# Kernel tuning notes

Hardware: AMD Instinct MI355X
Metric: run time of the kernel (lower is better)

The kernel has to match this reference:

```python
import jax, jax.numpy as jnp
import numpy as np

# Block-structured decompression constants (SFACTOR=2 on 32x32 channels)
RBLKS, CBLKS = 2, 2      # blocks per axis
RPIX, CPIX = 8, 8        # compressed block size
OUT_HW = 32              # decompressed channel size
B = 32768


def setup_inputs() -> dict:
    key = jax.random.key(0)
    k1, k2, k3, k4 = jax.random.split(key, 4)
    x = jax.random.normal(k1, (B, 3, 16, 16), dtype=jnp.float32)
    # per-row-block decompression matrices: [rblks, 2*RPIX, RPIX]
    lhs = jax.random.normal(k2, (RBLKS, 2 * RPIX, RPIX), dtype=jnp.float32) * 0.1
    # per-col-block decompression matrices: [cblks, CPIX, 2*CPIX]
    rhs = jax.random.normal(k3, (CBLKS, CPIX, 2 * CPIX), dtype=jnp.float32) * 0.1
    W = jax.random.normal(k4, (1, 3 * 32 * 32), dtype=jnp.float32) * 0.02
    b = jnp.zeros((1,), dtype=jnp.float32)
    return {"x": x, "lhs": lhs, "rhs": rhs, "W": W, "b": b}


def _decompress(xc, lhs, rhs):
    # xc: [B, 16, 16] compressed channel -> [B, 32, 32]
    n = xc.shape[0]
    # split into [B, rblk, RPIX, cblk, CPIX] blocks
    blocks = xc.reshape(n, RBLKS, RPIX, CBLKS, CPIX)
    # per-block: out_block = lhs[r] @ block @ rhs[c]  (block-wise bfloat16 decompression math)
    out = jnp.einsum('rPp,brpcq,cqQ->brPcQ', lhs, blocks, rhs)
    return out.reshape(n, OUT_HW, OUT_HW)


def reference(x, lhs, rhs, W, b):
    # three per-channel decompression calls, as in the original forward
    r = _decompress(x[:, 0], lhs, rhs)
    g = _decompress(x[:, 1], lhs, rhs)
    bch = _decompress(x[:, 2], lhs, rhs)
    out = jnp.stack((r, g, bch), axis=1)            # [B, 3, 32, 32]
    out = out.reshape(-1, 3 * 32 * 32)              # [B, 3072]
    return out @ W.T + b                            # [B, 1]
```

## Files before the change

kernel.cpp:

```cpp
#include <hip/hip_runtime.h>
#include <hip/hip_bf16.h>


#define BATCH 32768
#define ROW_F4 192
#define ROWS_PER_BLOCK 32
#define GRID_BLOCKS (BATCH / ROWS_PER_BLOCK)

__device__ __forceinline__ float dot4(const float4& a, const float4& b) {
    return a.x * b.x + a.y * b.y + a.z * b.z + a.w * b.w;
}

__device__ __forceinline__ void reduce2_store(float a0, float a1, int lane,
                                              float* __restrict__ outp,
                                              float bias) {
    a0 += __shfl_xor(a0, 1);
    a1 += __shfl_xor(a1, 1);
    float b = (lane & 1) ? a1 : a0;
    b += __shfl_xor(b, 2);
    b += __shfl_xor(b, 4);
    b += __shfl_xor(b, 8);
    b += __shfl_xor(b, 16);
    b += __shfl_xor(b, 32);
    if (lane < 2) outp[lane] = b + bias;
}

__global__ __launch_bounds__(256, 4) void fused_compressor_kernel(
        const float4* __restrict__ x4,
        const float4* __restrict__ lhs4,
        const float4* __restrict__ rhs4,
        const float4* __restrict__ W4,
        const float* __restrict__ bptr,
        float* __restrict__ out) {
    __shared__ __align__(16) float Wl[3072];
    __shared__ __align__(16) float rh[256];
    __shared__ __align__(16) float lh[256];
    __shared__ float tmp[1536];
    __shared__ __align__(16) float weff[768];

    const int tid  = threadIdx.x;
    const int lane = tid & 63;
    const int w    = tid >> 6;

    const int wrow = blockIdx.x * ROWS_PER_BLOCK + w * 8;

    const float4* xr = x4 + (size_t)wrow * ROW_F4 + lane;
    float4 xa[2][3], xb[2][3];
    #pragma unroll
    for (int r = 0; r < 2; ++r)
        #pragma unroll
        for (int k = 0; k < 3; ++k)
            xa[r][k] = xr[r * ROW_F4 + k * 64];
    #pragma unroll
    for (int r = 0; r < 2; ++r)
        #pragma unroll
        for (int k = 0; k < 3; ++k)
            xb[r][k] = xr[(2 + r) * ROW_F4 + k * 64];

    float4 wreg0 = W4[tid];
    float4 wreg1 = W4[tid + 256];
    float4 wreg2 = W4[tid + 512];
    int sidx = tid & 127;
    float4 sreg = (sidx < 64) ? rhs4[sidx] : lhs4[sidx - 64];

    reinterpret_cast<float4*>(Wl)[tid]       = wreg0;
    reinterpret_cast<float4*>(Wl)[tid + 256] = wreg1;
    reinterpret_cast<float4*>(Wl)[tid + 512] = wreg2;
    if (tid < 128) {
        if (tid < 64) reinterpret_cast<float4*>(rh)[tid] = sreg;
        else          reinterpret_cast<float4*>(lh)[tid - 64] = sreg;
    }
    __syncthreads();

    const float4* rhv = reinterpret_cast<const float4*>(rh);
    const float4* Wlv = reinterpret_cast<const float4*>(Wl);
    #pragma unroll
    for (int s = 0; s < 6; ++s) {
        int idx = tid + (s << 8);
        int ch  = idx >> 9;
        int rem = idx & 511;
        int R   = rem >> 4;
        int j   = rem & 15;
        int c   = j >> 3;
        int q   = j & 7;
        const float4* rp = rhv + c * 32 + q * 4;
        const float4* wp = Wlv + ch * 256 + R * 8 + c * 4;
        tmp[idx] = dot4(rp[0], wp[0]) + dot4(rp[1], wp[1])
                 + dot4(rp[2], wp[2]) + dot4(rp[3], wp[3]);
    }
    __syncthreads();

    #pragma unroll
    for (int s = 0; s < 3; ++s) {
        int idx = tid + (s << 8);
        int ch  = idx >> 8;
        int rem = idx & 255;
        int i   = rem >> 4;
        int j   = rem & 15;
        int r   = i >> 3;
        int p   = i & 7;
        const float* lp = lh + r * 128 + p;
        const float* tp = tmp + ch * 512 + r * 256 + j;
        float acc = 0.f;
        #pragma unroll
        for (int P = 0; P < 16; ++P) acc += lp[P * 8] * tp[P * 16];
        weff[idx] = acc;
    }
    __syncthreads();

    const float4* wv4 = reinterpret_cast<const float4*>(weff);
    const float4 wv0 = wv4[lane];
    const float4 wv1 = wv4[lane + 64];
    const float4 wv2 = wv4[lane + 128];
    const float  bias = bptr[0];

    {
        float a0 = dot4(xa[0][0], wv0) + dot4(xa[0][1], wv1) + dot4(xa[0][2], wv2);
        float a1 = dot4(xa[1][0], wv0) + dot4(xa[1][1], wv1) + dot4(xa[1][2], wv2);
        #pragma unroll
        for (int r = 0; r < 2; ++r)
            #pragma unroll
            for (int k = 0; k < 3; ++k)
                xa[r][k] = xr[(4 + r) * ROW_F4 + k * 64];
        reduce2_store(a0, a1, lane, out + wrow, bias);
    }
    {
        float a0 = dot4(xb[0][0], wv0) + dot4(xb[0][1], wv1) + dot4(xb[0][2], wv2);
        float a1 = dot4(xb[1][0], wv0) + dot4(xb[1][1], wv1) + dot4(xb[1][2], wv2);
        #pragma unroll
        for (int r = 0; r < 2; ++r)
            #pragma unroll
            for (int k = 0; k < 3; ++k)
                xb[r][k] = xr[(6 + r) * ROW_F4 + k * 64];
        reduce2_store(a0, a1, lane, out + wrow + 2, bias);
    }
    {
        float a0 = dot4(xa[0][0], wv0) + dot4(xa[0][1], wv1) + dot4(xa[0][2], wv2);
        float a1 = dot4(xa[1][0], wv0) + dot4(xa[1][1], wv1) + dot4(xa[1][2], wv2);
        reduce2_store(a0, a1, lane, out + wrow + 4, bias);
    }
    {
        float a0 = dot4(xb[0][0], wv0) + dot4(xb[0][1], wv1) + dot4(xb[0][2], wv2);
        float a1 = dot4(xb[1][0], wv0) + dot4(xb[1][1], wv1) + dot4(xb[1][2], wv2);
        reduce2_store(a0, a1, lane, out + wrow + 6, bias);
    }
}

extern "C" void kernel_launch(void* const* d_in, const int* in_sizes, int n_in,
                              void* d_out, int out_size, void* d_ws, size_t ws_size,
                              hipStream_t stream) {
    const float* x   = (const float*)d_in[0];
    const float* lhs = (const float*)d_in[1];
    const float* rhs = (const float*)d_in[2];
    const float* W   = (const float*)d_in[3];
    const float* b   = (const float*)d_in[4];
    float* out = (float*)d_out;

    fused_compressor_kernel<<<GRID_BLOCKS, 256, 0, stream>>>(
        (const float4*)x, (const float4*)lhs, (const float4*)rhs,
        (const float4*)W, b, out);
}
```

Measured before the change: 20.64 us.

## Load params via async LDS DMA and compute weights in one wave with flag

Weight and decompression-matrix staging now uses global_load_lds, direct global-to-LDS loads issued by wave 0, instead of going through registers. Wave 0 alone computes the effective weight vector. The other three waves spin on a volatile LDS flag rather than meeting at three block-wide barriers. The goal is to drop the register round-trip and the barrier costs so the x loads overlap the parameter setup. In exchange, one wave does four times the setup arithmetic on the critical path, and the waiting waves busy-spin and compete for issue slots. Correctness relies on the compiler inserting the wait for the LDS DMA before wave 0 reads the data.

Result: slower. 26.78 us (+29.7%).

```diff
diff --git a/kernel.cpp b/kernel.cpp
--- a/kernel.cpp
+++ b/kernel.cpp
@@ -7,8 +7,19 @@
 #define ROWS_PER_BLOCK 32
 #define GRID_BLOCKS (BATCH / ROWS_PER_BLOCK)
 
+#define PRM_W    0
+#define PRM_RHS  3072
+#define PRM_LHS  3328
+#define PRM_TOT  3584
+
 __device__ __forceinline__ float dot4(const float4& a, const float4& b) {
     return a.x * b.x + a.y * b.y + a.z * b.z + a.w * b.w;
+}
+
+__device__ __forceinline__ void async_lds16(const float* g, float* l) {
+    __builtin_amdgcn_global_load_lds(
+        (const __attribute__((address_space(1))) unsigned int*)g,
+        (__attribute__((address_space(3))) unsigned int*)l, 16, 0, 0);
 }
 
 __device__ __forceinline__ void reduce2_store(float a0, float a1, int lane,
@@ -25,24 +36,34 @@
     if (lane < 2) outp[lane] = b + bias;
 }
 
-__global__ __launch_bounds__(256, 4) void fused_compressor_kernel(
+__global__ __launch_bounds__(256, 4) void fused_pc_kernel(
         const float4* __restrict__ x4,
-        const float4* __restrict__ lhs4,
-        const float4* __restrict__ rhs4,
-        const float4* __restrict__ W4,
+        const float* __restrict__ lhsp,
+        const float* __restrict__ rhsp,
+        const float* __restrict__ Wp,
         const float* __restrict__ bptr,
         float* __restrict__ out) {
-    __shared__ __align__(16) float Wl[3072];
-    __shared__ __align__(16) float rh[256];
-    __shared__ __align__(16) float lh[256];
+    __shared__ __align__(16) float prm[PRM_TOT];
     __shared__ float tmp[1536];
     __shared__ __align__(16) float weff[768];
+    __shared__ int flag;
 
     const int tid  = threadIdx.x;
     const int lane = tid & 63;
     const int w    = tid >> 6;
+    const int wrow = blockIdx.x * ROWS_PER_BLOCK + w * 8;
 
-    const int wrow = blockIdx.x * ROWS_PER_BLOCK + w * 8;
+    if (tid == 0) flag = 0;
+    __syncthreads();
+
+    if (w == 0) {
+        #pragma unroll
+        for (int c = 0; c < 12; ++c)
+            async_lds16(Wp + c * 256 + lane * 4, prm + PRM_W + c * 256);
+        async_lds16(rhsp + lane * 4, prm + PRM_RHS);
+        async_lds16(lhsp + lane * 4, prm + PRM_LHS);
+    }
+    __builtin_amdgcn_sched_barrier(0);
 
     const float4* xr = x4 + (size_t)wrow * ROW_F4 + lane;
     float4 xa[2][3], xb[2][3];
@@ -56,59 +77,56 @@
         #pragma unroll
         for (int k = 0; k < 3; ++k)
             xb[r][k] = xr[(2 + r) * ROW_F4 + k * 64];
+    __builtin_amdgcn_sched_barrier(0);
 
-    float4 wreg0 = W4[tid];
-    float4 wreg1 = W4[tid + 256];
-    float4 wreg2 = W4[tid + 512];
-    int sidx = tid & 127;
-    float4 sreg = (sidx < 64) ? rhs4[sidx] : lhs4[sidx - 64];
+    volatile int* vflag = &flag;
+    const int g = lane >> 4;
+    const int j = lane & 15;
 
-    reinterpret_cast<float4*>(Wl)[tid]       = wreg0;
-    reinterpret_cast<float4*>(Wl)[tid + 256] = wreg1;
-    reinterpret_cast<float4*>(Wl)[tid + 512] = wreg2;
-    if (tid < 128) {
-        if (tid < 64) reinterpret_cast<float4*>(rh)[tid] = sreg;
-        else          reinterpret_cast<float4*>(lh)[tid - 64] = sreg;
+    if (w == 0) {
+        const float4* rhv = (const float4*)(prm + PRM_RHS);
+        const float4* Wlv = (const float4*)(prm + PRM_W);
+        const float*  lh  = prm + PRM_LHS;
+        const int c_ = j >> 3, q = j & 7;
+
+        const float4 rr0 = rhv[c_ * 32 + q * 4 + 0];
+        const float4 rr1 = rhv[c_ * 32 + q * 4 + 1];
+        const float4 rr2 = rhv[c_ * 32 + q * 4 + 2];
+        const float4 rr3 = rhv[c_ * 32 + q * 4 + 3];
+
+        #pragma unroll
+        for (int s = 0; s < 24; ++s) {
+            int v  = g + 4 * s;
+            int ch = v >> 5, R = v & 31;
+            const float4* wp = Wlv + ch * 256 + R * 8 + c_ * 4;
+            tmp[v * 16 + j] = dot4(rr0, wp[0]) + dot4(rr1, wp[1])
+                            + dot4(rr2, wp[2]) + dot4(rr3, wp[3]);
+        }
+
+        #pragma unroll
+        for (int ii = 0; ii < 4; ++ii) {
+            int i = g + 4 * ii;
+            int r = i >> 3, p = i & 7;
+            float lv[16];
+            #pragma unroll
+            for (int P = 0; P < 16; ++P) lv[P] = lh[r * 128 + P * 8 + p];
+            #pragma unroll
+            for (int ch = 0; ch < 3; ++ch) {
+                const float* tp = tmp + ch * 512 + r * 256 + j;
+                float acc = 0.f;
+                #pragma unroll
+                for (int P = 0; P < 16; ++P) acc += lv[P] * tp[P * 16];
+                weff[ch * 256 + i * 16 + j] = acc;
+            }
+        }
+        __threadfence_block();
+        if (lane == 0) *vflag = 1;
+    } else {
+        while (*vflag == 0) { }
+        __threadfence_block();
     }
-    __syncthreads();
 
-    const float4* rhv = reinterpret_cast<const float4*>(rh);
-    const float4* Wlv = reinterpret_cast<const float4*>(Wl);
-    #pragma unroll
-    for (int s = 0; s < 6; ++s) {
-        int idx = tid + (s << 8);
-        int ch  = idx >> 9;
-        int rem = idx & 511;
-        int R   = rem >> 4;
-        int j   = rem & 15;
-        int c   = j >> 3;
-        int q   = j & 7;
-        const float4* rp = rhv + c * 32 + q * 4;
-        const float4* wp = Wlv + ch * 256 + R * 8 + c * 4;
-        tmp[idx] = dot4(rp[0], wp[0]) + dot4(rp[1], wp[1])
-                 + dot4(rp[2], wp[2]) + dot4(rp[3], wp[3]);
-    }
-    __syncthreads();
-
-    #pragma unroll
-    for (int s = 0; s < 3; ++s) {
-        int idx = tid + (s << 8);
-        int ch  = idx >> 8;
-        int rem = idx & 255;
-        int i   = rem >> 4;
-        int j   = rem & 15;
-        int r   = i >> 3;
-        int p   = i & 7;
-        const float* lp = lh + r * 128 + p;
-        const float* tp = tmp + ch * 512 + r * 256 + j;
-        float acc = 0.f;
-        #pragma unroll
-        for (int P = 0; P < 16; ++P) acc += lp[P * 8] * tp[P * 16];
-        weff[idx] = acc;
-    }
-    __syncthreads();
-
-    const float4* wv4 = reinterpret_cast<const float4*>(weff);
+    const float4* wv4 = (const float4*)weff;
     const float4 wv0 = wv4[lane];
     const float4 wv1 = wv4[lane + 64];
     const float4 wv2 = wv4[lane + 128];
@@ -156,7 +174,6 @@
     const float* b   = (const float*)d_in[4];
     float* out = (float*)d_out;
 
-    fused_compressor_kernel<<<GRID_BLOCKS, 256, 0, stream>>>(
-        (const float4*)x, (const float4*)lhs, (const float4*)rhs,
-        (const float4*)W, b, out);
+    fused_pc_kernel<<<GRID_BLOCKS, 256, 0, stream>>>(
+        (const float4*)x, lhs, rhs, W, b, out);
 }
```
